# Kernel optimization log

Hardware: AMD Instinct MI355X
Metric: run time of the kernel (lower is better)

Reference implementation:

```python
import jax, jax.numpy as jnp
import numpy as np

B, F, P, K, C = 16384, 256, 16, 16, 2  # batch, fea_num, field_num, latent_dim, class_num


def setup_inputs() -> dict:
    key = jax.random.key(0)
    k1, k2, k3, k4 = jax.random.split(key, 4)
    x = jax.random.normal(k1, (B, F), dtype=jnp.float32)
    field_map = (jnp.arange(F, dtype=jnp.int32) % P).astype(jnp.int32)  # feature -> field
    W = jax.random.normal(k2, (C, F), dtype=jnp.float32) * 0.05
    b = jax.random.normal(k3, (C,), dtype=jnp.float32) * 0.05
    v = jax.random.normal(k4, (F, P, K, C), dtype=jnp.float32) * 0.05
    return {"x": x, "field_map": field_map, "W": W, "b": b, "v": v}


def reference(x, field_map, W, b, v):
    # G[i, j, k, c] = v[i, field(j), k, c]
    G = v[:, field_map]                                   # [F, F, K, C]
    # T[i, j, c] = sum_k v[i, f_j, k, c] * v[j, f_i, k, c]  (symmetric in i<->j)
    T = jnp.einsum('ijkc,jikc->ijc', G, G)                # [F, F, C]
    # sum_{i<j} x_i x_j T_ij = 0.5 * (sum_{i,j} x_i x_j T_ij - sum_i x_i^2 T_ii)
    Y = jnp.einsum('bi,ijc->bjc', x, T)                   # [B, F, C]
    full = jnp.einsum('bj,bjc->bc', x, Y)                 # [B, C]
    T_diag = jnp.einsum('iic->ic', T)                     # [F, C]
    diag = jnp.einsum('bi,ic->bc', x * x, T_diag)         # [B, C]
    interaction = 0.5 * (full - diag)
    linear_part = x @ W.T + b                             # [B, C]
    return jax.nn.log_softmax(linear_part + interaction, axis=1)
```

## Files before the change

### kernel.cpp

```cpp
#include <hip/hip_runtime.h>
#include <cstdint>

using bfrag = __attribute__((ext_vector_type(8))) short;
using sh4   = __attribute__((ext_vector_type(4))) short;
using f32x4 = __attribute__((ext_vector_type(4))) float;

__device__ __forceinline__ unsigned short f2bf(float f) {
    union { float f; unsigned int u; } z; z.f = f;
    unsigned int u = z.u;
    return (unsigned short)((u + 0x7FFFu + ((u >> 16) & 1u)) >> 16);
}
__device__ __forceinline__ float bf2f(unsigned short h) {
    union { unsigned int u; float f; } z; z.u = ((unsigned int)h) << 16;
    return z.f;
}

__global__ __launch_bounds__(256) void build_T(const float* __restrict__ v,
                                               unsigned short* __restrict__ TU) {
    __shared__ float va2[16 * 528];
    __shared__ float vb2[16 * 33];
    const int p = blockIdx.x >> 4, jq = blockIdx.x & 15;
    const int t = threadIdx.x;

    {
        const int m = t >> 4, s = t & 15;
        const float4* row = (const float4*)(v + (p + 16 * m) * 512);
#pragma unroll
        for (int e = 0; e < 8; ++e) {
            const int f4 = s + 16 * e;
            float4 u4 = row[f4];
            const int fi = f4 * 4;
            float* dst = &va2[m * 528 + (fi >> 5) * 33 + (fi & 31)];
            dst[0] = u4.x; dst[1] = u4.y; dst[2] = u4.z; dst[3] = u4.w;
        }
    }
    if (t < 128) {
        const int u = t >> 3, e = t & 7;
        float4 u4 = *(const float4*)(v + (jq * 16 + u) * 512 + p * 32 + e * 4);
        float* dst = &vb2[u * 33 + e * 4];
        dst[0] = u4.x; dst[1] = u4.y; dst[2] = u4.z; dst[3] = u4.w;
    }
    __syncthreads();

    const int m = t >> 4, u = t & 15;
    const int i = p + 16 * m, j = jq * 16 + u;
    float a0 = 0.f, a1 = 0.f;
#pragma unroll
    for (int k = 0; k < 16; ++k) {
        a0 += va2[m * 528 + u * 33 + 2 * k]     * vb2[u * 33 + 2 * k];
        a1 += va2[m * 528 + u * 33 + 2 * k + 1] * vb2[u * 33 + 2 * k + 1];
    }
    const unsigned short t0 = (j > i) ? f2bf(a0) : (unsigned short)0;
    const unsigned short t1 = (j > i) ? f2bf(a1) : (unsigned short)0;
    const int base = m * 4096 + (j >> 5) * 512 + (((j >> 3) & 3) * 16 + p) * 8 + (j & 7);
    TU[base]         = t0;
    TU[65536 + base] = t1;
}

__global__ __launch_bounds__(512) void ffm_main(const float* __restrict__ x,
                                                const float* __restrict__ W,
                                                const float* __restrict__ bias,
                                                const unsigned short* __restrict__ TU,
                                                float* __restrict__ out) {
    __shared__ __align__(16) unsigned short xs[64 * 256];
    __shared__ float Wld[512];
    __shared__ float4 fullpart[64][8];

    const int tid = threadIdx.x;
    const int wgrow = blockIdx.x * 64;

    {
        const int r = tid >> 3, h = tid & 7;
        const float4* gx = (const float4*)(x + (wgrow + r) * 256) + h * 8;
#pragma unroll
        for (int qp = 0; qp < 4; ++qp) {
            float4 u0 = gx[2 * qp], u1 = gx[2 * qp + 1];
            bfrag pk;
            pk[0] = (short)f2bf(u0.x); pk[1] = (short)f2bf(u0.y);
            pk[2] = (short)f2bf(u0.z); pk[3] = (short)f2bf(u0.w);
            pk[4] = (short)f2bf(u1.x); pk[5] = (short)f2bf(u1.y);
            pk[6] = (short)f2bf(u1.z); pk[7] = (short)f2bf(u1.w);
            const int cj = h * 4 + qp;
            *(bfrag*)(&xs[r * 256 + ((cj ^ (r & 7)) << 3)]) = pk;
        }
        Wld[tid] = W[tid];
    }
    __syncthreads();

    const int lane = tid & 63, cg = tid >> 6;
    const int lr = lane & 15, lg = lane >> 4;
    const int nbA = cg, nbB = 15 - cg;

    f32x4 acc[2][2][4];
#pragma unroll
    for (int s = 0; s < 2; ++s)
#pragma unroll
        for (int c = 0; c < 2; ++c)
#pragma unroll
            for (int mb = 0; mb < 4; ++mb)
                acc[s][c][mb] = (f32x4){0.f, 0.f, 0.f, 0.f};

#pragma unroll
    for (int ks = 0; ks < 8; ++ks) {
        bfrag bx[4];
#pragma unroll
        for (int mb = 0; mb < 4; ++mb) {
            const int b = mb * 16 + lr;
            const int cj = ks * 4 + lg;
            bx[mb] = *(const bfrag*)(&xs[b * 256 + ((cj ^ (b & 7)) << 3)]);
        }
        if (ks >= (nbA >> 1)) {
            bfrag at0 = *(const bfrag*)(TU + nbA * 4096 + ks * 512 + lane * 8);
            bfrag at1 = *(const bfrag*)(TU + 65536 + nbA * 4096 + ks * 512 + lane * 8);
#pragma unroll
            for (int mb = 0; mb < 4; ++mb) {
                acc[0][0][mb] = __builtin_amdgcn_mfma_f32_16x16x32_bf16(at0, bx[mb], acc[0][0][mb], 0, 0, 0);
                acc[0][1][mb] = __builtin_amdgcn_mfma_f32_16x16x32_bf16(at1, bx[mb], acc[0][1][mb], 0, 0, 0);
            }
        }
        if (ks >= (nbB >> 1)) {
            bfrag at0 = *(const bfrag*)(TU + nbB * 4096 + ks * 512 + lane * 8);
            bfrag at1 = *(const bfrag*)(TU + 65536 + nbB * 4096 + ks * 512 + lane * 8);
#pragma unroll
            for (int mb = 0; mb < 4; ++mb) {
                acc[1][0][mb] = __builtin_amdgcn_mfma_f32_16x16x32_bf16(at0, bx[mb], acc[1][0][mb], 0, 0, 0);
                acc[1][1][mb] = __builtin_amdgcn_mfma_f32_16x16x32_bf16(at1, bx[mb], acc[1][1][mb], 0, 0, 0);
            }
        }
    }

    float pi0[4], pi1[4], pl0[4], pl1[4];
#pragma unroll
    for (int mb = 0; mb < 4; ++mb) { pi0[mb] = pi1[mb] = pl0[mb] = pl1[mb] = 0.f; }

#pragma unroll
    for (int sel = 0; sel < 2; ++sel) {
        const int nb2 = sel ? nbB : nbA;
        const int jb = nb2 * 16 + lg * 4;
        const float w00 = Wld[jb], w01 = Wld[jb + 1], w02 = Wld[jb + 2], w03 = Wld[jb + 3];
        const float w10 = Wld[256 + jb], w11 = Wld[256 + jb + 1],
                    w12 = Wld[256 + jb + 2], w13 = Wld[256 + jb + 3];
#pragma unroll
        for (int mb = 0; mb < 4; ++mb) {
            const int b = mb * 16 + lr;
            sh4 xq = *(const sh4*)(&xs[b * 256 + (((jb >> 3) ^ (b & 7)) << 3) + (jb & 7)]);
            const float x0 = bf2f((unsigned short)xq[0]);
            const float x1 = bf2f((unsigned short)xq[1]);
            const float x2 = bf2f((unsigned short)xq[2]);
            const float x3 = bf2f((unsigned short)xq[3]);
            pi0[mb] += acc[sel][0][mb][0] * x0 + acc[sel][0][mb][1] * x1 +
                       acc[sel][0][mb][2] * x2 + acc[sel][0][mb][3] * x3;
            pi1[mb] += acc[sel][1][mb][0] * x0 + acc[sel][1][mb][1] * x1 +
                       acc[sel][1][mb][2] * x2 + acc[sel][1][mb][3] * x3;
            pl0[mb] += w00 * x0 + w01 * x1 + w02 * x2 + w03 * x3;
            pl1[mb] += w10 * x0 + w11 * x1 + w12 * x2 + w13 * x3;
        }
    }
#pragma unroll
    for (int mb = 0; mb < 4; ++mb) {
        pi0[mb] += __shfl_xor(pi0[mb], 16, 64); pi0[mb] += __shfl_xor(pi0[mb], 32, 64);
        pi1[mb] += __shfl_xor(pi1[mb], 16, 64); pi1[mb] += __shfl_xor(pi1[mb], 32, 64);
        pl0[mb] += __shfl_xor(pl0[mb], 16, 64); pl0[mb] += __shfl_xor(pl0[mb], 32, 64);
        pl1[mb] += __shfl_xor(pl1[mb], 16, 64); pl1[mb] += __shfl_xor(pl1[mb], 32, 64);
    }
    if (lg == 0) {
#pragma unroll
        for (int mb = 0; mb < 4; ++mb)
            fullpart[mb * 16 + lr][cg] = make_float4(pi0[mb], pi1[mb], pl0[mb], pl1[mb]);
    }
    __syncthreads();

    if (tid < 64) {
        float i0 = 0.f, i1 = 0.f, l0 = 0.f, l1 = 0.f;
#pragma unroll
        for (int g = 0; g < 8; ++g) {
            float4 f = fullpart[tid][g];
            i0 += f.x; i1 += f.y; l0 += f.z; l1 += f.w;
        }
        const float z0 = l0 + bias[0] + i0;
        const float z1 = l1 + bias[1] + i1;
        const float mz = fmaxf(z0, z1);
        const float lse = mz + logf(expf(z0 - mz) + expf(z1 - mz));
        out[(wgrow + tid) * 2 + 0] = z0 - lse;
        out[(wgrow + tid) * 2 + 1] = z1 - lse;
    }
}

extern "C" void kernel_launch(void* const* d_in, const int* in_sizes, int n_in,
                              void* d_out, int out_size, void* d_ws, size_t ws_size,
                              hipStream_t stream) {
    const float* x    = (const float*)d_in[0];
    const float* W    = (const float*)d_in[2];
    const float* bias = (const float*)d_in[3];
    const float* v    = (const float*)d_in[4];
    float* out = (float*)d_out;

    unsigned short* TU = (unsigned short*)d_ws;

    build_T<<<dim3(256), dim3(256), 0, stream>>>(v, TU);
    ffm_main<<<dim3(256), dim3(512), 0, stream>>>(x, W, bias, TU, out);
}
```

Before: 18.48 us.

## Remap build_T blocks to field pairs so each block loads only needed slices

The T-building kernel is re-indexed so each block covers one (field of i, field of j) pair, with i = 16m+p and j = 16n+q. Every j in a block then shares one field, so each block stages just two 16x32 slices of v instead of 16 full rows of v. This is meant to cut global and L2 traffic and LDS use in the preprocessing kernel. The tiles are padded to a stride of 36 floats, and the output layout of T is unchanged.

```diff
diff --git a/kernel.cpp b/kernel.cpp
--- a/kernel.cpp
+++ b/kernel.cpp
@@ -17,42 +17,36 @@
 
 __global__ __launch_bounds__(256) void build_T(const float* __restrict__ v,
                                                unsigned short* __restrict__ TU) {
-    __shared__ float va2[16 * 528];
-    __shared__ float vb2[16 * 33];
-    const int p = blockIdx.x >> 4, jq = blockIdx.x & 15;
+    __shared__ float va[16 * 36];
+    __shared__ float vb[16 * 36];
+    const int p = blockIdx.x >> 4, q = blockIdx.x & 15;
     const int t = threadIdx.x;
 
-    {
-        const int m = t >> 4, s = t & 15;
-        const float4* row = (const float4*)(v + (p + 16 * m) * 512);
-#pragma unroll
-        for (int e = 0; e < 8; ++e) {
-            const int f4 = s + 16 * e;
-            float4 u4 = row[f4];
-            const int fi = f4 * 4;
-            float* dst = &va2[m * 528 + (fi >> 5) * 33 + (fi & 31)];
-            dst[0] = u4.x; dst[1] = u4.y; dst[2] = u4.z; dst[3] = u4.w;
-        }
-    }
     if (t < 128) {
-        const int u = t >> 3, e = t & 7;
-        float4 u4 = *(const float4*)(v + (jq * 16 + u) * 512 + p * 32 + e * 4);
-        float* dst = &vb2[u * 33 + e * 4];
+        const int m = t >> 3, e = t & 7;
+        float4 u4 = *(const float4*)(v + (16 * m + p) * 512 + q * 32 + 4 * e);
+        float* dst = &va[m * 36 + 4 * e];
+        dst[0] = u4.x; dst[1] = u4.y; dst[2] = u4.z; dst[3] = u4.w;
+    } else {
+        const int n = (t - 128) >> 3, e = t & 7;
+        float4 u4 = *(const float4*)(v + (16 * n + q) * 512 + p * 32 + 4 * e);
+        float* dst = &vb[n * 36 + 4 * e];
         dst[0] = u4.x; dst[1] = u4.y; dst[2] = u4.z; dst[3] = u4.w;
     }
     __syncthreads();
 
-    const int m = t >> 4, u = t & 15;
-    const int i = p + 16 * m, j = jq * 16 + u;
+    const int m = t >> 4, n = t & 15;
+    const int i = 16 * m + p, j = 16 * n + q;
     float a0 = 0.f, a1 = 0.f;
 #pragma unroll
     for (int k = 0; k < 16; ++k) {
-        a0 += va2[m * 528 + u * 33 + 2 * k]     * vb2[u * 33 + 2 * k];
-        a1 += va2[m * 528 + u * 33 + 2 * k + 1] * vb2[u * 33 + 2 * k + 1];
+        a0 += va[m * 36 + 2 * k]     * vb[n * 36 + 2 * k];
+        a1 += va[m * 36 + 2 * k + 1] * vb[n * 36 + 2 * k + 1];
     }
     const unsigned short t0 = (j > i) ? f2bf(a0) : (unsigned short)0;
     const unsigned short t1 = (j > i) ? f2bf(a1) : (unsigned short)0;
-    const int base = m * 4096 + (j >> 5) * 512 + (((j >> 3) & 3) * 16 + p) * 8 + (j & 7);
+    const int base = m * 4096 + (j >> 5) * 512 +
+                     (((j >> 3) & 3) * 16 + p) * 8 + (j & 7);
     TU[base]         = t0;
     TU[65536 + base] = t1;
 }
```

After: 18.23 us, median of 4. About the same (-1.3%).
